# Kernel optimization log

Hardware: AMD Instinct MI355X
Metric: run time of the kernel (lower is better)

Reference implementation:

```python
import jax, jax.numpy as jnp
import numpy as np

B, N, E, H = 8, 2048, 1024, 16
D = E // H

def setup_inputs() -> dict:
    key = jax.random.key(0)
    kx, kw1, kb1, kw2, kb2 = jax.random.split(key, 5)
    scale = 0.02
    return {
        "x": jax.random.normal(kx, (B, N, E), dtype=jnp.float32),
        "Wqkv": jax.random.normal(kw1, (3 * E, E), dtype=jnp.float32) * scale,
        "bqkv": jax.random.normal(kb1, (3 * E,), dtype=jnp.float32) * scale,
        "Wo": jax.random.normal(kw2, (E, E), dtype=jnp.float32) * scale,
        "bo": jax.random.normal(kb2, (E,), dtype=jnp.float32) * scale,
    }

def reference(x, Wqkv, bqkv, Wo, bo):
    b, n, e = x.shape
    h, d = H, D
    # qkv projection: torch Linear is x @ W.T + b
    qkv = x @ Wqkv.T + bqkv                                   # [B,N,3E]
    qkv = qkv.reshape(b, n, 3, h, d).transpose(2, 0, 3, 1, 4)  # [3,B,H,N,D]
    q, k, v = qkv[0], qkv[1], qkv[2]                           # each [B,H,N,D]
    # NOTE: replicates the original's einsum labeling exactly: with q,k of
    # shape [B,H,N,D], 'nqhd,nkhd->nhqk' contracts over D and yields [B,N,H,H]
    # (softmax over the head axis), matching the torch source bit-for-bit.
    energy = jnp.einsum('nqhd,nkhd->nhqk', q, k)               # [B,N,H,H]
    attention = jax.nn.softmax(energy / jnp.sqrt(jnp.float32(e)), axis=-1)
    out = jnp.einsum('nhql,nlhd->nqhd', attention, v)          # [B,H,N,D]
    out = out.reshape(b, n, e)                                 # same raw-buffer reshape as torch
    return out @ Wo.T + bo
```

## Files before the change

kernel.cpp:

```cpp
#include <hip/hip_runtime.h>
#include <hip/hip_bf16.h>
#include <stdint.h>


typedef __attribute__((ext_vector_type(8))) short short8;
typedef __attribute__((ext_vector_type(8))) unsigned short ushort8;
typedef __attribute__((ext_vector_type(16))) float floatx16;

__device__ __forceinline__ unsigned short f2bf(float f) {
  union { float f; uint32_t u; } x; x.f = f;
  uint32_t u = x.u;
  return (unsigned short)((u + 0x7fffu + ((u >> 16) & 1u)) >> 16);
}
__device__ __forceinline__ float bf2f(unsigned short s) {
  union { uint32_t u; float f; } x; x.u = ((uint32_t)s) << 16; return x.f;
}

__global__ __launch_bounds__(256) void cvt_kernel(const float* __restrict__ in,
                                                  unsigned short* __restrict__ out, int n8) {
  int i = blockIdx.x * 256 + threadIdx.x;
  if (i >= n8) return;
  long base = (long)i * 8;
  const float4* p = (const float4*)(in + base);
  float4 a = p[0], b = p[1];
  ushort8 r;
  r[0] = f2bf(a.x); r[1] = f2bf(a.y); r[2] = f2bf(a.z); r[3] = f2bf(a.w);
  r[4] = f2bf(b.x); r[5] = f2bf(b.y); r[6] = f2bf(b.z); r[7] = f2bf(b.w);
  *(ushort8*)(out + base) = r;
}

__device__ __forceinline__ void gl2lds16(const void* g, void* l) {
  __builtin_amdgcn_global_load_lds(
      (const uint32_t __attribute__((address_space(1)))*)g,
      (uint32_t __attribute__((address_space(3)))*)(uint32_t)(uintptr_t)l,
      16, 0, 0);
}

template <bool OUT_BF16>
__device__ __forceinline__ void gemm_core(const unsigned short* __restrict__ A,
                                          const unsigned short* __restrict__ Bm,
                                          const float* __restrict__ bias,
                                          void* __restrict__ Cout, int N, int K) {
  __shared__ __align__(16) unsigned short lA[128 * 64];
  __shared__ __align__(16) unsigned short lB[128 * 64];
  const int tid = threadIdx.x;
  const int lane = tid & 63;
  const int wave = tid >> 6;
  const long row0 = (long)blockIdx.y * 128;
  const long col0 = (long)blockIdx.x * 128;
  const int wr = (wave & 1) * 64;
  const int wc = (wave >> 1) * 64;
  const int l32 = lane & 31;
  const int lhi = lane >> 5;
  const int l7 = lane & 7;

  floatx16 acc[2][2] = {};

  const int rstage = tid >> 3;
  const int cstage = (tid & 7) ^ (rstage & 7);
  const unsigned short* gA0 = A + (row0 + rstage) * (long)K + cstage * 8;
  const unsigned short* gB0 = Bm + (col0 + rstage) * (long)K + cstage * 8;
  char* ldsA0 = (char*)lA + tid * 16;
  char* ldsB0 = (char*)lB + tid * 16;
  const long rowstep = (long)32 * K;

  int aRow[2], bRow[2], sOff[4];
#pragma unroll
  for (int i = 0; i < 2; i++) aRow[i] = (wr + i * 32 + l32) * 128;
#pragma unroll
  for (int j = 0; j < 2; j++) bRow[j] = (wc + j * 32 + l32) * 128;
#pragma unroll
  for (int s = 0; s < 4; s++) sOff[s] = ((2 * s + lhi) ^ l7) * 16;

  for (int k0 = 0; k0 < K; k0 += 64) {
    __syncthreads();
#pragma unroll
    for (int p = 0; p < 4; p++) {
      gl2lds16(gA0 + p * rowstep + k0, ldsA0 + p * 4096);
      gl2lds16(gB0 + p * rowstep + k0, ldsB0 + p * 4096);
    }
    __syncthreads();

#pragma unroll
    for (int s = 0; s < 4; s++) {
      short8 a0 = *(const short8*)((char*)lA + aRow[0] + sOff[s]);
      short8 a1 = *(const short8*)((char*)lA + aRow[1] + sOff[s]);
      short8 b0 = *(const short8*)((char*)lB + bRow[0] + sOff[s]);
      short8 b1 = *(const short8*)((char*)lB + bRow[1] + sOff[s]);
      acc[0][0] = __builtin_amdgcn_mfma_f32_32x32x16_bf16(a0, b0, acc[0][0], 0, 0, 0);
      acc[0][1] = __builtin_amdgcn_mfma_f32_32x32x16_bf16(a0, b1, acc[0][1], 0, 0, 0);
      acc[1][0] = __builtin_amdgcn_mfma_f32_32x32x16_bf16(a1, b0, acc[1][0], 0, 0, 0);
      acc[1][1] = __builtin_amdgcn_mfma_f32_32x32x16_bf16(a1, b1, acc[1][1], 0, 0, 0);
    }
  }

  float bv[2];
#pragma unroll
  for (int j = 0; j < 2; j++) bv[j] = bias[col0 + wc + j * 32 + l32];

#pragma unroll
  for (int i = 0; i < 2; i++) {
#pragma unroll
    for (int j = 0; j < 2; j++) {
      const long col = col0 + wc + j * 32 + l32;
      const long rbase = row0 + wr + i * 32 + 4 * lhi;
#pragma unroll
      for (int reg = 0; reg < 16; reg++) {
        const long row = rbase + (reg & 3) + 8 * (reg >> 2);
        float v = acc[i][j][reg] + bv[j];
        if (OUT_BF16)
          ((unsigned short*)Cout)[row * N + col] = f2bf(v);
        else
          ((float*)Cout)[row * N + col] = v;
      }
    }
  }
}

__global__ __launch_bounds__(256) void gemm_qkv(const unsigned short* __restrict__ A,
                                                const unsigned short* __restrict__ Bm,
                                                const float* __restrict__ bias,
                                                unsigned short* __restrict__ Cout,
                                                int N, int K) {
  gemm_core<true>(A, Bm, bias, Cout, N, K);
}

__global__ __launch_bounds__(256) void gemm_out(const unsigned short* __restrict__ A,
                                                const unsigned short* __restrict__ Bm,
                                                const float* __restrict__ bias,
                                                float* __restrict__ Cout,
                                                int N, int K) {
  gemm_core<false>(A, Bm, bias, Cout, N, K);
}

__global__ __launch_bounds__(256) void attn_kernel(const unsigned short* __restrict__ qkv,
                                                   unsigned short* __restrict__ out2) {
  const int t = blockIdx.x * 256 + threadIdx.x;
  const int head = t & 15;
  const int token = t >> 4;
  const int b = token >> 11;
  const int s = token & 2047;
  const unsigned short* base = qkv + (long)token * 3072;

  float qf[64];
  {
    const uint4* qp = (const uint4*)(base + head * 64);
#pragma unroll
    for (int w = 0; w < 8; w++) {
      uint4 u = qp[w];
      uint32_t arr[4] = {u.x, u.y, u.z, u.w};
#pragma unroll
      for (int c = 0; c < 4; c++) {
        qf[w * 8 + c * 2 + 0] = bf2f((unsigned short)(arr[c] & 0xffffu));
        qf[w * 8 + c * 2 + 1] = bf2f((unsigned short)(arr[c] >> 16));
      }
    }
  }

  float e[16];
  const unsigned short* kbase = base + 1024;
  for (int j = 0; j < 16; j++) {
    const uint4* kp = (const uint4*)(kbase + j * 64);
    float acc = 0.f;
#pragma unroll
    for (int w = 0; w < 8; w++) {
      uint4 u = kp[w];
      uint32_t arr[4] = {u.x, u.y, u.z, u.w};
#pragma unroll
      for (int c = 0; c < 4; c++) {
        acc += qf[w * 8 + c * 2 + 0] * bf2f((unsigned short)(arr[c] & 0xffffu));
        acc += qf[w * 8 + c * 2 + 1] * bf2f((unsigned short)(arr[c] >> 16));
      }
    }
    e[j] = acc * 0.03125f;
  }

  float mx = e[0];
#pragma unroll
  for (int j = 1; j < 16; j++) mx = fmaxf(mx, e[j]);
  float p[16];
  float sum = 0.f;
#pragma unroll
  for (int j = 0; j < 16; j++) { p[j] = __expf(e[j] - mx); sum += p[j]; }
  const float inv = 1.f / sum;

  float o[64];
#pragma unroll
  for (int d = 0; d < 64; d++) o[d] = 0.f;
  const unsigned short* vbase = base + 2048;
  for (int j = 0; j < 16; j++) {
    const float wgt = p[j] * inv;
    const uint4* vp = (const uint4*)(vbase + j * 64);
#pragma unroll
    for (int w = 0; w < 8; w++) {
      uint4 u = vp[w];
      uint32_t arr[4] = {u.x, u.y, u.z, u.w};
#pragma unroll
      for (int c = 0; c < 4; c++) {
        o[w * 8 + c * 2 + 0] += wgt * bf2f((unsigned short)(arr[c] & 0xffffu));
        o[w * 8 + c * 2 + 1] += wgt * bf2f((unsigned short)(arr[c] >> 16));
      }
    }
  }

  const long row = (long)b * 2048 + head * 128 + (s >> 4);
  unsigned short* op = out2 + row * 1024 + (long)(s & 15) * 64;
#pragma unroll
  for (int w = 0; w < 8; w++) {
    ushort8 r;
#pragma unroll
    for (int c = 0; c < 8; c++) r[c] = f2bf(o[w * 8 + c]);
    *(ushort8*)(op + w * 8) = r;
  }
}

extern "C" void kernel_launch(void* const* d_in, const int* in_sizes, int n_in,
                              void* d_out, int out_size, void* d_ws, size_t ws_size,
                              hipStream_t stream) {
  const float* x    = (const float*)d_in[0];
  const float* Wqkv = (const float*)d_in[1];
  const float* bqkv = (const float*)d_in[2];
  const float* Wo   = (const float*)d_in[3];
  const float* bo   = (const float*)d_in[4];
  float* out = (float*)d_out;

  char* ws = (char*)d_ws;
  unsigned short* x_bf    = (unsigned short*)(ws);
  unsigned short* wqkv_bf = (unsigned short*)(ws + 33554432);
  unsigned short* wo_bf   = (unsigned short*)(ws + 39845888);
  unsigned short* qkv_bf  = (unsigned short*)(ws + 41943040);
  unsigned short* out2_bf = (unsigned short*)(ws + 142606336);

  cvt_kernel<<<8192, 256, 0, stream>>>(x, x_bf, 16777216 / 8);
  cvt_kernel<<<1536, 256, 0, stream>>>(Wqkv, wqkv_bf, 3145728 / 8);
  cvt_kernel<<<512, 256, 0, stream>>>(Wo, wo_bf, 1048576 / 8);

  dim3 g1(3072 / 128, 16384 / 128);
  gemm_qkv<<<g1, 256, 0, stream>>>(x_bf, wqkv_bf, bqkv, qkv_bf, 3072, 1024);

  attn_kernel<<<1024, 256, 0, stream>>>(qkv_bf, out2_bf);

  dim3 g2(1024 / 128, 16384 / 128);
  gemm_out<<<g2, 256, 0, stream>>>(out2_bf, wo_bf, bo, out, 1024, 1024);
}
```

Baseline: 357.8 us.

## Widen GEMM tiles to 128x256, fuse conversions, unroll attention loops

The GEMM block tile grows from 128x128 to 128x256, with each wave computing a 64x128 sub-tile. This doubles B-operand reuse per A load and halves the number of blocks, at the cost of more accumulator registers and LDS (launch_bounds 256,2). The three fp32-to-bf16 conversion launches are merged into one kernel that picks its source by index, saving launch overhead. In the attention kernel the head loops are fully unrolled and the QK dot product is split across four partial accumulators to shorten dependency chains.

Result: slower. 602.8 us (+68.5%).

```diff
diff --git a/kernel.cpp b/kernel.cpp
--- a/kernel.cpp
+++ b/kernel.cpp
@@ -16,17 +16,29 @@
   union { uint32_t u; float f; } x; x.u = ((uint32_t)s) << 16; return x.f;
 }
 
-__global__ __launch_bounds__(256) void cvt_kernel(const float* __restrict__ in,
-                                                  unsigned short* __restrict__ out, int n8) {
+__global__ __launch_bounds__(256) void cvt_all(const float* __restrict__ x,
+                                               const float* __restrict__ w1,
+                                               const float* __restrict__ w2,
+                                               unsigned short* __restrict__ xb,
+                                               unsigned short* __restrict__ w1b,
+                                               unsigned short* __restrict__ w2b) {
   int i = blockIdx.x * 256 + threadIdx.x;
-  if (i >= n8) return;
+  const float* src;
+  unsigned short* dst;
+  if (i < 2097152) {
+    src = x; dst = xb;
+  } else if (i < 2097152 + 393216) {
+    i -= 2097152; src = w1; dst = w1b;
+  } else {
+    i -= 2490368; src = w2; dst = w2b;
+  }
   long base = (long)i * 8;
-  const float4* p = (const float4*)(in + base);
+  const float4* p = (const float4*)(src + base);
   float4 a = p[0], b = p[1];
   ushort8 r;
   r[0] = f2bf(a.x); r[1] = f2bf(a.y); r[2] = f2bf(a.z); r[3] = f2bf(a.w);
   r[4] = f2bf(b.x); r[5] = f2bf(b.y); r[6] = f2bf(b.z); r[7] = f2bf(b.w);
-  *(ushort8*)(out + base) = r;
+  *(ushort8*)(dst + base) = r;
 }
 
 __device__ __forceinline__ void gl2lds16(const void* g, void* l) {
@@ -42,19 +54,19 @@
                                           const float* __restrict__ bias,
                                           void* __restrict__ Cout, int N, int K) {
   __shared__ __align__(16) unsigned short lA[128 * 64];
-  __shared__ __align__(16) unsigned short lB[128 * 64];
+  __shared__ __align__(16) unsigned short lB[256 * 64];
   const int tid = threadIdx.x;
   const int lane = tid & 63;
   const int wave = tid >> 6;
   const long row0 = (long)blockIdx.y * 128;
-  const long col0 = (long)blockIdx.x * 128;
-  const int wr = (wave & 1) * 64;
-  const int wc = (wave >> 1) * 64;
+  const long col0 = (long)blockIdx.x * 256;
+  const int wr = (wave >> 1) * 64;
+  const int wc = (wave & 1) * 128;
   const int l32 = lane & 31;
   const int lhi = lane >> 5;
   const int l7 = lane & 7;
 
-  floatx16 acc[2][2] = {};
+  floatx16 acc[2][4] = {};
 
   const int rstage = tid >> 3;
   const int cstage = (tid & 7) ^ (rstage & 7);
@@ -64,21 +76,22 @@
   char* ldsB0 = (char*)lB + tid * 16;
   const long rowstep = (long)32 * K;
 
-  int aRow[2], bRow[2], sOff[4];
+  int aRow[2], bRow[4], sOff[4];
 #pragma unroll
   for (int i = 0; i < 2; i++) aRow[i] = (wr + i * 32 + l32) * 128;
 #pragma unroll
-  for (int j = 0; j < 2; j++) bRow[j] = (wc + j * 32 + l32) * 128;
+  for (int j = 0; j < 4; j++) bRow[j] = (wc + j * 32 + l32) * 128;
 #pragma unroll
   for (int s = 0; s < 4; s++) sOff[s] = ((2 * s + lhi) ^ l7) * 16;
 
   for (int k0 = 0; k0 < K; k0 += 64) {
     __syncthreads();
 #pragma unroll
-    for (int p = 0; p < 4; p++) {
+    for (int p = 0; p < 4; p++)
       gl2lds16(gA0 + p * rowstep + k0, ldsA0 + p * 4096);
+#pragma unroll
+    for (int p = 0; p < 8; p++)
       gl2lds16(gB0 + p * rowstep + k0, ldsB0 + p * 4096);
-    }
     __syncthreads();
 
 #pragma unroll
@@ -87,21 +100,27 @@
       short8 a1 = *(const short8*)((char*)lA + aRow[1] + sOff[s]);
       short8 b0 = *(const short8*)((char*)lB + bRow[0] + sOff[s]);
       short8 b1 = *(const short8*)((char*)lB + bRow[1] + sOff[s]);
+      short8 b2 = *(const short8*)((char*)lB + bRow[2] + sOff[s]);
+      short8 b3 = *(const short8*)((char*)lB + bRow[3] + sOff[s]);
       acc[0][0] = __builtin_amdgcn_mfma_f32_32x32x16_bf16(a0, b0, acc[0][0], 0, 0, 0);
       acc[0][1] = __builtin_amdgcn_mfma_f32_32x32x16_bf16(a0, b1, acc[0][1], 0, 0, 0);
+      acc[0][2] = __builtin_amdgcn_mfma_f32_32x32x16_bf16(a0, b2, acc[0][2], 0, 0, 0);
+      acc[0][3] = __builtin_amdgcn_mfma_f32_32x32x16_bf16(a0, b3, acc[0][3], 0, 0, 0);
       acc[1][0] = __builtin_amdgcn_mfma_f32_32x32x16_bf16(a1, b0, acc[1][0], 0, 0, 0);
       acc[1][1] = __builtin_amdgcn_mfma_f32_32x32x16_bf16(a1, b1, acc[1][1], 0, 0, 0);
-    }
-  }
-
-  float bv[2];
-#pragma unroll
-  for (int j = 0; j < 2; j++) bv[j] = bias[col0 + wc + j * 32 + l32];
+      acc[1][2] = __builtin_amdgcn_mfma_f32_32x32x16_bf16(a1, b2, acc[1][2], 0, 0, 0);
+      acc[1][3] = __builtin_amdgcn_mfma_f32_32x32x16_bf16(a1, b3, acc[1][3], 0, 0, 0);
+    }
+  }
+
+  float bv[4];
+#pragma unroll
+  for (int j = 0; j < 4; j++) bv[j] = bias[col0 + wc + j * 32 + l32];
 
 #pragma unroll
   for (int i = 0; i < 2; i++) {
 #pragma unroll
-    for (int j = 0; j < 2; j++) {
+    for (int j = 0; j < 4; j++) {
       const long col = col0 + wc + j * 32 + l32;
       const long rbase = row0 + wr + i * 32 + 4 * lhi;
 #pragma unroll
@@ -117,19 +136,19 @@
   }
 }
 
-__global__ __launch_bounds__(256) void gemm_qkv(const unsigned short* __restrict__ A,
-                                                const unsigned short* __restrict__ Bm,
-                                                const float* __restrict__ bias,
-                                                unsigned short* __restrict__ Cout,
-                                                int N, int K) {
+__global__ __launch_bounds__(256, 2) void gemm_qkv(const unsigned short* __restrict__ A,
+                                                   const unsigned short* __restrict__ Bm,
+                                                   const float* __restrict__ bias,
+                                                   unsigned short* __restrict__ Cout,
+                                                   int N, int K) {
   gemm_core<true>(A, Bm, bias, Cout, N, K);
 }
 
-__global__ __launch_bounds__(256) void gemm_out(const unsigned short* __restrict__ A,
-                                                const unsigned short* __restrict__ Bm,
-                                                const float* __restrict__ bias,
-                                                float* __restrict__ Cout,
-                                                int N, int K) {
+__global__ __launch_bounds__(256, 2) void gemm_out(const unsigned short* __restrict__ A,
+                                                   const unsigned short* __restrict__ Bm,
+                                                   const float* __restrict__ bias,
+                                                   float* __restrict__ Cout,
+                                                   int N, int K) {
   gemm_core<false>(A, Bm, bias, Cout, N, K);
 }
 
@@ -159,20 +178,24 @@
 
   float e[16];
   const unsigned short* kbase = base + 1024;
+#pragma unroll
   for (int j = 0; j < 16; j++) {
     const uint4* kp = (const uint4*)(kbase + j * 64);
-    float acc = 0.f;
+    float a0 = 0.f, a1 = 0.f, a2 = 0.f, a3 = 0.f;
 #pragma unroll
     for (int w = 0; w < 8; w++) {
       uint4 u = kp[w];
       uint32_t arr[4] = {u.x, u.y, u.z, u.w};
-#pragma unroll
-      for (int c = 0; c < 4; c++) {
-        acc += qf[w * 8 + c * 2 + 0] * bf2f((unsigned short)(arr[c] & 0xffffu));
-        acc += qf[w * 8 + c * 2 + 1] * bf2f((unsigned short)(arr[c] >> 16));
-      }
-    }
-    e[j] = acc * 0.03125f;
+      a0 += qf[w * 8 + 0] * bf2f((unsigned short)(arr[0] & 0xffffu));
+      a0 += qf[w * 8 + 1] * bf2f((unsigned short)(arr[0] >> 16));
+      a1 += qf[w * 8 + 2] * bf2f((unsigned short)(arr[1] & 0xffffu));
+      a1 += qf[w * 8 + 3] * bf2f((unsigned short)(arr[1] >> 16));
+      a2 += qf[w * 8 + 4] * bf2f((unsigned short)(arr[2] & 0xffffu));
+      a2 += qf[w * 8 + 5] * bf2f((unsigned short)(arr[2] >> 16));
+      a3 += qf[w * 8 + 6] * bf2f((unsigned short)(arr[3] & 0xffffu));
+      a3 += qf[w * 8 + 7] * bf2f((unsigned short)(arr[3] >> 16));
+    }
+    e[j] = ((a0 + a1) + (a2 + a3)) * 0.03125f;
   }
 
   float mx = e[0];
@@ -188,6 +211,7 @@
 #pragma unroll
   for (int d = 0; d < 64; d++) o[d] = 0.f;
   const unsigned short* vbase = base + 2048;
+#pragma unroll
   for (int j = 0; j < 16; j++) {
     const float wgt = p[j] * inv;
     const uint4* vp = (const uint4*)(vbase + j * 64);
@@ -231,15 +255,13 @@
   unsigned short* qkv_bf  = (unsigned short*)(ws + 41943040);
   unsigned short* out2_bf = (unsigned short*)(ws + 142606336);
 
-  cvt_kernel<<<8192, 256, 0, stream>>>(x, x_bf, 16777216 / 8);
-  cvt_kernel<<<1536, 256, 0, stream>>>(Wqkv, wqkv_bf, 3145728 / 8);
-  cvt_kernel<<<512, 256, 0, stream>>>(Wo, wo_bf, 1048576 / 8);
-
-  dim3 g1(3072 / 128, 16384 / 128);
+  cvt_all<<<10240, 256, 0, stream>>>(x, Wqkv, Wo, x_bf, wqkv_bf, wo_bf);
+
+  dim3 g1(3072 / 256, 16384 / 128);
   gemm_qkv<<<g1, 256, 0, stream>>>(x_bf, wqkv_bf, bqkv, qkv_bf, 3072, 1024);
 
   attn_kernel<<<1024, 256, 0, stream>>>(qkv_bf, out2_bf);
 
-  dim3 g2(1024 / 128, 16384 / 128);
+  dim3 g2(1024 / 256, 16384 / 128);
   gemm_out<<<g2, 256, 0, stream>>>(out2_bf, wo_bf, bo, out, 1024, 1024);
 }
```
